# Performance work log

Hardware: AMD Instinct MI355X
Metric: run time of the kernel (lower is better)

The kernel has to match this reference:

```python
import jax, jax.numpy as jnp
import numpy as np


def mesa_head(xh, yh, qh, lam):
    # xh = per-head 'inputs' (v_proj output), yh = 'targets' (k_proj output),
    # qh = queries; all [T, d]. lam is this head's scalar lambda.
    T, d = xh.shape
    init_inv = jnp.eye(d, dtype=xh.dtype) * lam

    def step(inv, tok):
        x_t, q_t = tok
        Hx = inv @ x_t                      # [d]   (cur_inverse @ x)
        xH = x_t @ inv                      # [d]   (x^T @ cur_inverse)
        denom = 1.0 + x_t @ Hx              # scalar: forward=1 + x^T H x
        new_inv = inv - jnp.outer(Hx, xH) / denom   # Sherman-Morrison rank-1 update
        return new_inv, new_inv @ q_t       # pred_t = S_t @ q_t

    _, preds = jax.lax.scan(step, init_inv, (xh, qh))  # preds: [T, d]

    # scaled_dot_product_attention(preds, xh, yh) with masked=True,
    # use_softmax=False, normalization=False: tril-masked linear attention.
    logits = preds @ xh.T                               # [T, T]
    mask = jnp.tril(jnp.ones((T, T), dtype=bool))
    logits = jnp.where(mask, logits, jnp.zeros((), dtype=logits.dtype))
    return logits @ yh                                  # [T, d]


def reference(x, Wq, Wk, Wv, Wo, lambdas):
    B, T, E = x.shape
    H = lambdas.shape[0]
    d = Wq.shape[1] // H
    q = (x @ Wq).reshape(B, T, H, d)   # query_heads
    k = (x @ Wk).reshape(B, T, H, d)   # target_heads
    v = (x @ Wv).reshape(B, T, H, d)   # input_heads
    # Original call: mesa(input_heads, target_heads, query_heads, lambdas, norm)
    over_batch = jax.vmap(mesa_head, in_axes=(0, 0, 0, None))
    over_heads = jax.vmap(over_batch, in_axes=(2, 2, 2, 0), out_axes=-1)
    mesa_out = over_heads(v, k, q, lambdas)             # [B, T, d, H]
    # Faithful to original: reshape combines (d, H) in that order before o_proj.
    out = mesa_out.reshape(B, T, H * d) @ Wo            # [B, T, E]
    return out


def setup_inputs() -> dict:
    key = jax.random.key(0)
    ks = jax.random.split(key, 6)
    B, T, E, H, d = 2, 1024, 512, 8, 64
    s_in = 1.0 / np.sqrt(E).astype(np.float32)
    s_out = 1.0 / np.sqrt(H * d).astype(np.float32)
    return {
        "x": jax.random.normal(ks[0], (B, T, E), dtype=jnp.float32),
        "Wq": jax.random.normal(ks[1], (E, H * d), dtype=jnp.float32) * s_in,
        "Wk": jax.random.normal(ks[2], (E, H * d), dtype=jnp.float32) * s_in,
        "Wv": jax.random.normal(ks[3], (E, H * d), dtype=jnp.float32) * s_in,
        "Wo": jax.random.normal(ks[4], (H * d, E), dtype=jnp.float32) * s_out,
        "lambdas": jnp.ones((H,), dtype=jnp.float32),
    }
```

## Files before the change

kernel.cpp:

```cpp
#include <hip/hip_runtime.h>

#define T_SEQ 1024
#define DH 64
#define NH 8
#define NB 2
#define EMB 512
#define CS 32
#define NCH 32
#define ACH 16
#define NCHAIN 16

typedef __attribute__((ext_vector_type(8))) short bf16x8;
typedef __attribute__((ext_vector_type(4))) float f32x4;

__device__ __forceinline__ int swz4(int r, int c4) {
    return r * 16 + ((c4 ^ (r >> 2)) & 15);
}

__device__ __forceinline__ void fma4(float4& o, float s, const float4& b) {
    o.x += s * b.x; o.y += s * b.y; o.z += s * b.z; o.w += s * b.w;
}

__device__ __forceinline__ ushort f2bf(float f) {
    unsigned u = __float_as_uint(f);
    return (ushort)((u + 0x7FFFu + ((u >> 16) & 1u)) >> 16);
}
__device__ __forceinline__ float bf2f(ushort h) {
    return __uint_as_float(((unsigned)h) << 16);
}
__device__ __forceinline__ void split2(float f, ushort& hi, ushort& lo) {
    hi = f2bf(f);
    lo = f2bf(f - bf2f(hi));
}

__global__ __launch_bounds__(256) void prep_qkv(
    const float* __restrict__ x, const float* __restrict__ W0,
    const float* __restrict__ W1, const float* __restrict__ W2,
    ushort* __restrict__ x_hi, ushort* __restrict__ x_lo,
    ushort* __restrict__ Wt_hi, ushort* __restrict__ Wt_lo) {
    int zz = blockIdx.z;
    int t = threadIdx.x;
    __shared__ float T[64][65];
    if (zz < 3) {
        const float* W = (zz == 0) ? W0 : (zz == 1) ? W1 : W2;
        ushort* hi = Wt_hi + (size_t)zz * 262144;
        ushort* lo = Wt_lo + (size_t)zz * 262144;
        int kk0 = blockIdx.x * 64, n0 = blockIdx.y * 64;
#pragma unroll
        for (int i = 0; i < 4; ++i) {
            int rl = i * 16 + (t >> 4);
            float4 vv = *(const float4*)&W[(size_t)(kk0 + rl) * 512 + n0 + (t & 15) * 4];
            T[rl][(t & 15) * 4 + 0] = vv.x;
            T[rl][(t & 15) * 4 + 1] = vv.y;
            T[rl][(t & 15) * 4 + 2] = vv.z;
            T[rl][(t & 15) * 4 + 3] = vv.w;
        }
        __syncthreads();
        int nl = t >> 2, kl = (t & 3) * 16;
#pragma unroll
        for (int j4 = 0; j4 < 4; ++j4) {
            ushort4 h4, l4;
            split2(T[kl + j4 * 4 + 0][nl], h4.x, l4.x);
            split2(T[kl + j4 * 4 + 1][nl], h4.y, l4.y);
            split2(T[kl + j4 * 4 + 2][nl], h4.z, l4.z);
            split2(T[kl + j4 * 4 + 3][nl], h4.w, l4.w);
            size_t dst = (size_t)(n0 + nl) * 512 + kk0 + kl + j4 * 4;
            *(ushort4*)&hi[dst] = h4;
            *(ushort4*)&lo[dst] = l4;
        }
    } else {
        int bid = blockIdx.y * 8 + blockIdx.x;
        const float4* in = (const float4*)x;
        ushort4* hi = (ushort4*)x_hi;
        ushort4* lo = (ushort4*)x_lo;
#pragma unroll
        for (int i = 0; i < 16; ++i) {
            int id = (bid * 16 + i) * 256 + t;
            float4 xv = in[id];
            ushort4 h, l;
            split2(xv.x, h.x, l.x);
            split2(xv.y, h.y, l.y);
            split2(xv.z, h.z, l.z);
            split2(xv.w, h.w, l.w);
            hi[id] = h;
            lo[id] = l;
        }
    }
}

__global__ __launch_bounds__(256) void prep_out(
    const float* __restrict__ Wo, const float4* __restrict__ ao,
    ushort* __restrict__ Wot_hi, ushort* __restrict__ Wot_lo,
    ushort4* __restrict__ A2_hi, ushort4* __restrict__ A2_lo) {
    int t = threadIdx.x;
    __shared__ float T[64][65];
    if (blockIdx.z == 0) {
        int kk0 = blockIdx.x * 64, n0 = blockIdx.y * 64;
#pragma unroll
        for (int i = 0; i < 4; ++i) {
            int rl = i * 16 + (t >> 4);
            int rs = rl * 8 + (kk0 >> 6);
            float4 vv = *(const float4*)&Wo[(size_t)rs * 512 + n0 + (t & 15) * 4];
            T[rl][(t & 15) * 4 + 0] = vv.x;
            T[rl][(t & 15) * 4 + 1] = vv.y;
            T[rl][(t & 15) * 4 + 2] = vv.z;
            T[rl][(t & 15) * 4 + 3] = vv.w;
        }
        __syncthreads();
        int nl = t >> 2, kl = (t & 3) * 16;
#pragma unroll
        for (int j4 = 0; j4 < 4; ++j4) {
            ushort4 h4, l4;
            split2(T[kl + j4 * 4 + 0][nl], h4.x, l4.x);
            split2(T[kl + j4 * 4 + 1][nl], h4.y, l4.y);
            split2(T[kl + j4 * 4 + 2][nl], h4.z, l4.z);
            split2(T[kl + j4 * 4 + 3][nl], h4.w, l4.w);
            size_t dst = (size_t)(n0 + nl) * 512 + kk0 + kl + j4 * 4;
            *(ushort4*)&Wot_hi[dst] = h4;
            *(ushort4*)&Wot_lo[dst] = l4;
        }
    } else {
        int bid = blockIdx.y * 8 + blockIdx.x;
#pragma unroll
        for (int i = 0; i < 16; ++i) {
            int id = (bid * 16 + i) * 256 + t;
            int chain = id >> 14;
            int tt = (id >> 4) & 1023;
            int d4 = id & 15;
            float4 xv = ao[id];
            int mrow = ((chain >> 3) << 10) + tt;
            int dst = mrow * 128 + ((chain & 7) << 4) + d4;
            ushort4 h, l;
            split2(xv.x, h.x, l.x);
            split2(xv.y, h.y, l.y);
            split2(xv.z, h.z, l.z);
            split2(xv.w, h.w, l.w);
            A2_hi[dst] = h;
            A2_lo[dst] = l;
        }
    }
}

template <int MODE>
__global__ __launch_bounds__(256) void mfma_gemm(
    const ushort* __restrict__ Ahi, const ushort* __restrict__ Alo,
    const ushort* __restrict__ Bth, const ushort* __restrict__ Btl,
    float* __restrict__ o0, float* __restrict__ o1, float* __restrict__ o2) {
    int bm = blockIdx.x, bn = blockIdx.y, zz = blockIdx.z;
    const ushort* Bh = Bth + (size_t)zz * 262144;
    const ushort* Bl = Btl + (size_t)zz * 262144;
    float* out = (MODE == 0) ? ((zz == 0) ? o0 : (zz == 1) ? o1 : o2) : o0;

    __shared__ ushort Ash[128 * 40];
    __shared__ ushort Asl[128 * 40];
    __shared__ ushort Bsh[64 * 40];
    __shared__ ushort Bsl[64 * 40];

    int tid = threadIdx.x;
    int lane = tid & 63, wid = tid >> 6;
    int wm = wid >> 1, wn = wid & 1;
    int fr = lane & 15, fk = (lane >> 4) * 8;
    int sr = tid >> 2, sc = (tid & 3) * 8;

    f32x4 zero = {0.f, 0.f, 0.f, 0.f};
    f32x4 acc[4][2];
#pragma unroll
    for (int f = 0; f < 4; ++f)
#pragma unroll
        for (int g = 0; g < 2; ++g) acc[f][g] = zero;

    const ushort* gAh = Ahi + (size_t)(bm * 128 + sr) * 512 + sc;
    const ushort* gAl = Alo + (size_t)(bm * 128 + sr) * 512 + sc;
    const ushort* gBh = Bh + (size_t)(bn * 64 + sr) * 512 + sc;
    const ushort* gBl = Bl + (size_t)(bn * 64 + sr) * 512 + sc;

    for (int k0 = 0; k0 < 512; k0 += 32) {
        uint4 a0 = *(const uint4*)(gAh + k0);
        uint4 a1 = *(const uint4*)(gAh + 64 * 512 + k0);
        uint4 a2 = *(const uint4*)(gAl + k0);
        uint4 a3 = *(const uint4*)(gAl + 64 * 512 + k0);
        uint4 b0 = *(const uint4*)(gBh + k0);
        uint4 b1 = *(const uint4*)(gBl + k0);
        __syncthreads();
        *(uint4*)&Ash[sr * 40 + sc] = a0;
        *(uint4*)&Ash[(sr + 64) * 40 + sc] = a1;
        *(uint4*)&Asl[sr * 40 + sc] = a2;
        *(uint4*)&Asl[(sr + 64) * 40 + sc] = a3;
        *(uint4*)&Bsh[sr * 40 + sc] = b0;
        *(uint4*)&Bsl[sr * 40 + sc] = b1;
        __syncthreads();
        bf16x8 ah[4], al[4], bh[2], blo[2];
#pragma unroll
        for (int f = 0; f < 4; ++f) {
            int r = wm * 64 + f * 16 + fr;
            ah[f] = *(const bf16x8*)&Ash[r * 40 + fk];
            al[f] = *(const bf16x8*)&Asl[r * 40 + fk];
        }
#pragma unroll
        for (int g = 0; g < 2; ++g) {
            int r = wn * 32 + g * 16 + fr;
            bh[g] = *(const bf16x8*)&Bsh[r * 40 + fk];
            blo[g] = *(const bf16x8*)&Bsl[r * 40 + fk];
        }
#pragma unroll
        for (int f = 0; f < 4; ++f)
#pragma unroll
            for (int g = 0; g < 2; ++g) {
                acc[f][g] = __builtin_amdgcn_mfma_f32_16x16x32_bf16(
                    ah[f], bh[g], acc[f][g], 0, 0, 0);
                acc[f][g] = __builtin_amdgcn_mfma_f32_16x16x32_bf16(
                    ah[f], blo[g], acc[f][g], 0, 0, 0);
                acc[f][g] = __builtin_amdgcn_mfma_f32_16x16x32_bf16(
                    al[f], bh[g], acc[f][g], 0, 0, 0);
            }
    }

    int rbase = (lane >> 4) * 4;
#pragma unroll
    for (int f = 0; f < 4; ++f)
#pragma unroll
        for (int g = 0; g < 2; ++g)
#pragma unroll
            for (int j = 0; j < 4; ++j) {
                int m = bm * 128 + wm * 64 + f * 16 + rbase + j;
                int n = bn * 64 + wn * 32 + g * 16 + (lane & 15);
                float val = acc[f][g][j];
                if (MODE == 0) {
                    int b = m >> 10, tt = m & 1023;
                    int h = n >> 6, d = n & 63;
                    out[(((size_t)(b * 8 + h) * 1024 + tt) << 6) + d] = val;
                } else {
                    out[(size_t)m * 512 + n] = val;
                }
            }
}

__global__ __launch_bounds__(256) void gram_kernel(
    const float* __restrict__ v, float* __restrict__ g) {
    int chain = blockIdx.x, chunk = blockIdx.y;
    const float* X = v + ((size_t)chain * T_SEQ + chunk * CS) * DH;
    __shared__ float Xs[CS * 64];
    int tid = threadIdx.x;
#pragma unroll
    for (int i = 0; i < (CS * 16) / 256; ++i)
        ((float4*)Xs)[i * 256 + tid] = ((const float4*)X)[i * 256 + tid];
    __syncthreads();

    int tx = tid & 15, ty = tid >> 4;
    float acc[4][4];
#pragma unroll
    for (int i = 0; i < 4; ++i)
#pragma unroll
        for (int j = 0; j < 4; ++j) acc[i][j] = 0.f;

#pragma unroll 4
    for (int t = 0; t < CS; ++t) {
        float a_[4], b_[4];
#pragma unroll
        for (int i = 0; i < 4; ++i) a_[i] = Xs[t * 64 + ty * 4 + i];
#pragma unroll
        for (int j = 0; j < 4; ++j) b_[j] = Xs[t * 64 + tx * 4 + j];
#pragma unroll
        for (int i = 0; i < 4; ++i)
#pragma unroll
            for (int j = 0; j < 4; ++j) acc[i][j] += a_[i] * b_[j];
    }

    float* gp = g + ((size_t)chain * NCH + chunk) * 4096;
#pragma unroll
    for (int i = 0; i < 4; ++i)
        *(float4*)(gp + (ty * 4 + i) * 64 + tx * 4) =
            make_float4(acc[i][0], acc[i][1], acc[i][2], acc[i][3]);
}

__global__ __launch_bounds__(256) void prefix_kernel(float* __restrict__ g) {
    int gid = blockIdx.x * 256 + threadIdx.x;
    int chain = gid >> 12, elem = gid & 4095;
    float* p = g + (size_t)chain * NCH * 4096 + elem;
    float vals[NCH];
#pragma unroll
    for (int c = 0; c < NCH; ++c) vals[c] = p[(size_t)c * 4096];
    float run = 0.f;
#pragma unroll
    for (int c = 0; c < NCH; ++c) {
        float t = vals[c];
        vals[c] = run;
        run += t;
    }
#pragma unroll
    for (int c = 0; c < NCH; ++c) p[(size_t)c * 4096] = vals[c];
}

__global__ __launch_bounds__(256) void invscan(
    const float* __restrict__ g, const float* __restrict__ v,
    const float* __restrict__ q, const float* __restrict__ lambdas,
    float* __restrict__ preds) {
    int blk = blockIdx.x;
    int chain = blk >> 5, chunk = blk & 31;
    int tid = threadIdx.x;
    int row = tid >> 2, ch = tid & 3, wav = tid >> 6;
    float lam = lambdas[chain & (NH - 1)];

    __shared__ float rbuf[2][64];
    __shared__ float sbuf[2][64];
    __shared__ float Xs[CS * 64];
    __shared__ float Qs[CS * 64];
    __shared__ float Po[CS * 64];
    __shared__ float red[2][6][4];

    float m[16];
    {
        const float4* gp = (const float4*)(g + ((size_t)chain * NCH + chunk) * 4096);
#pragma unroll
        for (int i = 0; i < 4; ++i) {
            float4 t4 = gp[row * 16 + ch * 4 + i];
            m[i * 4 + 0] = t4.x; m[i * 4 + 1] = t4.y;
            m[i * 4 + 2] = t4.z; m[i * 4 + 3] = t4.w;
        }
    }
#pragma unroll
    for (int i = 0; i < 16; ++i)
        if (ch * 16 + i == row) m[i] += lam;

    const float4* vb = (const float4*)(v + ((size_t)chain * T_SEQ + chunk * CS) * DH);
    const float4* qb = (const float4*)(q + ((size_t)chain * T_SEQ + chunk * CS) * DH);
    ((float4*)Xs)[tid] = vb[tid];
    ((float4*)Xs)[256 + tid] = vb[256 + tid];
    ((float4*)Qs)[tid] = qb[tid];
    ((float4*)Qs)[256 + tid] = qb[256 + tid];

    if (row == 0) {
#pragma unroll
        for (int i = 0; i < 4; ++i)
            ((float4*)rbuf[0])[ch * 4 + i] =
                make_float4(m[i * 4], m[i * 4 + 1], m[i * 4 + 2], m[i * 4 + 3]);
    }
    if (row == 1) {
#pragma unroll
        for (int i = 0; i < 4; ++i)
            ((float4*)sbuf[0])[ch * 4 + i] =
                make_float4(m[i * 4], m[i * 4 + 1], m[i * 4 + 2], m[i * 4 + 3]);
    }
    __syncthreads();

    const int colbase = ch * 16;

    for (int pp = 0; pp < 32; ++pp) {
        const int p = 2 * pp;
        const float* rb = rbuf[pp & 1];
        const float* sb = sbuf[pp & 1];
        float r_[16], s_[16];
#pragma unroll
        for (int i = 0; i < 4; ++i) {
            float4 t4 = ((const float4*)rb)[ch * 4 + i];
            r_[i * 4] = t4.x; r_[i * 4 + 1] = t4.y;
            r_[i * 4 + 2] = t4.z; r_[i * 4 + 3] = t4.w;
            float4 u4 = ((const float4*)sb)[ch * 4 + i];
            s_[i * 4] = u4.x; s_[i * 4 + 1] = u4.y;
            s_[i * 4 + 2] = u4.z; s_[i * 4 + 3] = u4.w;
        }
        float rp = rb[p], rp2 = rb[p + 1], sp2 = sb[p + 1];
        float gr = rb[row], gs = sb[row];
        float i1 = 1.f / rp;
        float al = rp2 * i1;
        float i2 = 1.f / (sp2 - al * rp2);
        float c0, ca, cb;
        if (row == p) {
            c0 = 0.f; ca = i1 + al * al * i2; cb = -al * i2;
        } else if (row == p + 1) {
            c0 = 0.f; ca = -al * i2; cb = i2;
        } else {
            float b2 = (gs - al * gr) * i2;
            c0 = 1.f; ca = al * b2 - gr * i1; cb = -b2;
        }
#pragma unroll
        for (int i = 0; i < 16; ++i) {
            float upd = c0 * m[i] + ca * r_[i] + cb * s_[i];
            int col = colbase + i;
            upd = (col == p) ? -ca : upd;
            upd = (col == p + 1) ? -cb : upd;
            m[i] = upd;
        }
        if (pp < 31) {
            if (row == p + 2) {
#pragma unroll
                for (int i = 0; i < 4; ++i)
                    ((float4*)rbuf[(pp + 1) & 1])[ch * 4 + i] =
                        make_float4(m[i * 4], m[i * 4 + 1], m[i * 4 + 2], m[i * 4 + 3]);
            }
            if (row == p + 3) {
#pragma unroll
                for (int i = 0; i < 4; ++i)
                    ((float4*)sbuf[(pp + 1) & 1])[ch * 4 + i] =
                        make_float4(m[i * 4], m[i * 4 + 1], m[i * 4 + 2], m[i * 4 + 3]);
            }
        }
        __syncthreads();
    }

    for (int tp = 0; tp < 16; ++tp) {
        const int ta = 2 * tp, tb2 = 2 * tp + 1;
        const int par = tp & 1;
        float pu = 0.f, pw = 0.f, pza = 0.f, pzb = 0.f;
#pragma unroll
        for (int i = 0; i < 4; ++i) {
            float4 xa = ((const float4*)(Xs + ta * 64))[ch * 4 + i];
            float4 xb = ((const float4*)(Xs + tb2 * 64))[ch * 4 + i];
            float4 qa = ((const float4*)(Qs + ta * 64))[ch * 4 + i];
            float4 q4 = ((const float4*)(Qs + tb2 * 64))[ch * 4 + i];
            pu += m[i * 4] * xa.x + m[i * 4 + 1] * xa.y + m[i * 4 + 2] * xa.z + m[i * 4 + 3] * xa.w;
            pw += m[i * 4] * xb.x + m[i * 4 + 1] * xb.y + m[i * 4 + 2] * xb.z + m[i * 4 + 3] * xb.w;
            pza += m[i * 4] * qa.x + m[i * 4 + 1] * qa.y + m[i * 4 + 2] * qa.z + m[i * 4 + 3] * qa.w;
            pzb += m[i * 4] * q4.x + m[i * 4 + 1] * q4.y + m[i * 4 + 2] * q4.z + m[i * 4 + 3] * q4.w;
        }
        pu += __shfl_xor(pu, 1); pu += __shfl_xor(pu, 2);
        pw += __shfl_xor(pw, 1); pw += __shfl_xor(pw, 2);
        pza += __shfl_xor(pza, 1); pza += __shfl_xor(pza, 2);
        pzb += __shfl_xor(pzb, 1); pzb += __shfl_xor(pzb, 2);
        float u = -pu, w = -pw, za = -pza, zb = -pzb;
        if (ch == 0) rbuf[par][row] = u;
        if (ch == 1) sbuf[par][row] = w;
        float a_ = Xs[ta * 64 + row], b_ = Xs[tb2 * 64 + row];
        float qa_ = Qs[ta * 64 + row], qb_ = Qs[tb2 * 64 + row];
        float d0 = a_ * u, d1 = b_ * u, d2 = b_ * w;
        float d3 = qa_ * u, d4 = qb_ * u, d5 = qb_ * w;
#pragma unroll
        for (int off = 32; off; off >>= 1) {
            d0 += __shfl_xor(d0, off); d1 += __shfl_xor(d1, off);
            d2 += __shfl_xor(d2, off); d3 += __shfl_xor(d3, off);
            d4 += __shfl_xor(d4, off); d5 += __shfl_xor(d5, off);
        }
        if ((tid & 63) == 0) {
            red[par][0][wav] = d0; red[par][1][wav] = d1; red[par][2][wav] = d2;
            red[par][3][wav] = d3; red[par][4][wav] = d4; red[par][5][wav] = d5;
        }
        __syncthreads();
        float saa = 0.25f * (red[par][0][0] + red[par][0][1] + red[par][0][2] + red[par][0][3]);
        float sab = 0.25f * (red[par][1][0] + red[par][1][1] + red[par][1][2] + red[par][1][3]);
        float sbb = 0.25f * (red[par][2][0] + red[par][2][1] + red[par][2][2] + red[par][2][3]);
        float c1  = 0.25f * (red[par][3][0] + red[par][3][1] + red[par][3][2] + red[par][3][3]);
        float c2  = 0.25f * (red[par][4][0] + red[par][4][1] + red[par][4][2] + red[par][4][3]);
        float c3  = 0.25f * (red[par][5][0] + red[par][5][1] + red[par][5][2] + red[par][5][3]);
        float k1 = 1.f / (1.f + saa);
        float al2 = sab * k1;
        float k2 = 1.f / (1.f + sbb - sab * al2);
        float vr = w - al2 * u;
        if (ch == 0) Po[ta * 64 + row] = za - (c1 * k1) * u;
        if (ch == 1) Po[tb2 * 64 + row] = zb - (c2 * k1) * u - (k2 * (c3 - al2 * c2)) * vr;
        float cu = k1 * u - al2 * k2 * vr;
        float cw = k2 * vr;
#pragma unroll
        for (int i = 0; i < 4; ++i) {
            float4 uj = ((const float4*)rbuf[par])[ch * 4 + i];
            float4 wj = ((const float4*)sbuf[par])[ch * 4 + i];
            m[i * 4 + 0] += cu * uj.x + cw * wj.x;
            m[i * 4 + 1] += cu * uj.y + cw * wj.y;
            m[i * 4 + 2] += cu * uj.z + cw * wj.z;
            m[i * 4 + 3] += cu * uj.w + cw * wj.w;
        }
    }
    __syncthreads();

    float4* po4 = (float4*)(preds + ((size_t)chain * T_SEQ + chunk * CS) * DH);
    po4[tid] = ((const float4*)Po)[tid];
    po4[256 + tid] = ((const float4*)Po)[256 + tid];
}

__global__ __launch_bounds__(256) void kv_gram(
    const float* __restrict__ V, const float* __restrict__ Kv,
    float* __restrict__ D) {
    int chain = blockIdx.x, ck = blockIdx.y;
    __shared__ float Vs[64 * 64];
    __shared__ float Ks2[64 * 64];
    int tid = threadIdx.x;
    const float4* Vb = (const float4*)(V + ((size_t)chain * T_SEQ + ck * 64) * DH);
    const float4* Kb = (const float4*)(Kv + ((size_t)chain * T_SEQ + ck * 64) * DH);
#pragma unroll
    for (int i = 0; i < 4; ++i) {
        ((float4*)Vs)[i * 256 + tid] = Vb[i * 256 + tid];
        ((float4*)Ks2)[i * 256 + tid] = Kb[i * 256 + tid];
    }
    __syncthreads();

    int tx = tid & 15, ty = tid >> 4;
    float acc[4][4];
#pragma unroll
    for (int i = 0; i < 4; ++i)
#pragma unroll
        for (int j = 0; j < 4; ++j) acc[i][j] = 0.f;

#pragma unroll 4
    for (int t = 0; t < 64; ++t) {
        float a_[4], b_[4];
#pragma unroll
        for (int i = 0; i < 4; ++i) a_[i] = Vs[t * 64 + ty * 4 + i];
#pragma unroll
        for (int j = 0; j < 4; ++j) b_[j] = Ks2[t * 64 + tx * 4 + j];
#pragma unroll
        for (int i = 0; i < 4; ++i)
#pragma unroll
            for (int j = 0; j < 4; ++j) acc[i][j] += a_[i] * b_[j];
    }

    float* dp = D + ((size_t)chain * ACH + ck) * 4096;
#pragma unroll
    for (int i = 0; i < 4; ++i)
        *(float4*)(dp + (ty * 4 + i) * 64 + tx * 4) =
            make_float4(acc[i][0], acc[i][1], acc[i][2], acc[i][3]);
}

__global__ __launch_bounds__(256) void kv_prefix(float* __restrict__ d) {
    int gid = blockIdx.x * 256 + threadIdx.x;
    int chain = gid >> 12, elem = gid & 4095;
    float* p = d + (size_t)chain * ACH * 4096 + elem;
    float vals[ACH];
#pragma unroll
    for (int c = 0; c < ACH; ++c) vals[c] = p[(size_t)c * 4096];
    float run = 0.f;
#pragma unroll
    for (int c = 0; c < ACH; ++c) {
        float t = vals[c];
        vals[c] = run;
        run += t;
    }
#pragma unroll
    for (int c = 0; c < ACH; ++c) p[(size_t)c * 4096] = vals[c];
}

__global__ __launch_bounds__(256) void attn_chunk(
    const float* __restrict__ P, const float* __restrict__ V,
    const float* __restrict__ Kv, const float* __restrict__ C,
    float* __restrict__ O) {
    int ck = blockIdx.x, bh = blockIdx.y;
    int tid = threadIdx.x, tx = tid & 15, ty = tid >> 4;

    __shared__ float4 Ps[64 * 16];
    __shared__ float4 Bs[64 * 16];
    __shared__ float4 Ks[64 * 16];

    int lr = tid >> 2, lc = tid & 3;
    const float4* Pb = (const float4*)(P + ((size_t)bh * T_SEQ + ck * 64) * DH);
    const float4* Vb = (const float4*)(V + ((size_t)bh * T_SEQ + ck * 64) * DH);
    const float4* Kb = (const float4*)(Kv + ((size_t)bh * T_SEQ + ck * 64) * DH);
    const float4* Cb = (const float4*)(C + ((size_t)bh * ACH + ck) * 4096);
#pragma unroll
    for (int i = 0; i < 4; ++i) {
        Ps[swz4(lr, lc + i * 4)] = Pb[lr * 16 + lc + i * 4];
        Bs[swz4(lr, lc + i * 4)] = Cb[lr * 16 + lc + i * 4];
        Ks[swz4(lr, lc + i * 4)] = Kb[lr * 16 + lc + i * 4];
    }

    float4 o[4];
    o[0] = o[1] = o[2] = o[3] = make_float4(0.f, 0.f, 0.f, 0.f);
    __syncthreads();

    const float* Pf = (const float*)Ps;
#pragma unroll 4
    for (int j = 0; j < 64; ++j) {
        float4 b4 = Bs[swz4(j, tx)];
#pragma unroll
        for (int i = 0; i < 4; ++i) {
            float s = Pf[swz4(ty * 4 + i, j >> 2) * 4 + (j & 3)];
            fma4(o[i], s, b4);
        }
    }
    __syncthreads();

#pragma unroll
    for (int i = 0; i < 4; ++i)
        Bs[swz4(lr, lc + i * 4)] = Vb[lr * 16 + lc + i * 4];
    __syncthreads();

    float4 sa[4][4];
#pragma unroll
    for (int i = 0; i < 4; ++i)
#pragma unroll
        for (int j = 0; j < 4; ++j) sa[i][j] = make_float4(0.f, 0.f, 0.f, 0.f);
#pragma unroll
    for (int d4 = 0; d4 < 16; ++d4) {
        float4 a[4], b[4];
#pragma unroll
        for (int i = 0; i < 4; ++i) a[i] = Ps[swz4(ty * 4 + i, d4)];
#pragma unroll
        for (int j = 0; j < 4; ++j) b[j] = Bs[swz4(tx * 4 + j, d4)];
#pragma unroll
        for (int i = 0; i < 4; ++i)
#pragma unroll
            for (int j = 0; j < 4; ++j) {
                sa[i][j].x += a[i].x * b[j].x;
                sa[i][j].y += a[i].y * b[j].y;
                sa[i][j].z += a[i].z * b[j].z;
                sa[i][j].w += a[i].w * b[j].w;
            }
    }
    __syncthreads();

#pragma unroll
    for (int i = 0; i < 4; ++i) {
        int m = ty * 4 + i;
        float sv[4];
#pragma unroll
        for (int j = 0; j < 4; ++j) {
            float s = sa[i][j].x + sa[i][j].y + sa[i][j].z + sa[i][j].w;
            if ((tx * 4 + j) > m) s = 0.f;
            sv[j] = s;
        }
        Bs[swz4(m, tx)] = make_float4(sv[0], sv[1], sv[2], sv[3]);
    }
    __syncthreads();

    const float* Sf = (const float*)Bs;
#pragma unroll 4
    for (int j = 0; j < 64; ++j) {
        float4 b4 = Ks[swz4(j, tx)];
#pragma unroll
        for (int i = 0; i < 4; ++i) {
            float s = Sf[swz4(ty * 4 + i, j >> 2) * 4 + (j & 3)];
            fma4(o[i], s, b4);
        }
    }

#pragma unroll
    for (int i = 0; i < 4; ++i) {
        float* dst = O + ((size_t)bh * T_SEQ + ck * 64 + ty * 4 + i) * DH + tx * 4;
        *(float4*)dst = o[i];
    }
}

extern "C" void kernel_launch(void* const* d_in, const int* in_sizes, int n_in,
                              void* d_out, int out_size, void* d_ws, size_t ws_size,
                              hipStream_t stream) {
    const float* x = (const float*)d_in[0];
    const float* Wq = (const float*)d_in[1];
    const float* Wk = (const float*)d_in[2];
    const float* Wv = (const float*)d_in[3];
    const float* Wo = (const float*)d_in[4];
    const float* lambdas = (const float*)d_in[5];
    float* out = (float*)d_out;

    float* ws = (float*)d_ws;
    const size_t SZ = (size_t)NB * NH * T_SEQ * DH;
    float* q = ws;
    float* k = ws + SZ;
    float* v = ws + 2 * SZ;
    float* preds = ws + 3 * SZ;
    ushort* x_hi = (ushort*)(ws + 3 * SZ);
    ushort* x_lo = (ushort*)(ws + 3 * SZ + SZ / 2);
    ushort* A2_hi = x_hi;
    ushort* A2_lo = x_lo;
    float* g = ws + 4 * SZ;
    ushort* Wt_hi = (ushort*)(ws + 4 * SZ);
    ushort* Wt_lo = (ushort*)(ws + 4 * SZ + 393216);
    float* dbuf = g;
    float* ao = g + SZ;
    ushort* Wot_hi = (ushort*)(ws + 4 * SZ);
    ushort* Wot_lo = (ushort*)(ws + 4 * SZ + 131072);

    prep_qkv<<<dim3(8, 8, 4), 256, 0, stream>>>(x, Wq, Wk, Wv,
                                                x_hi, x_lo, Wt_hi, Wt_lo);
    mfma_gemm<0><<<dim3(16, 8, 3), 256, 0, stream>>>(
        x_hi, x_lo, Wt_hi, Wt_lo, q, k, v);
    gram_kernel<<<dim3(NCHAIN, NCH), 256, 0, stream>>>(v, g);
    prefix_kernel<<<dim3(256), 256, 0, stream>>>(g);
    invscan<<<dim3(NCHAIN * NCH), 256, 0, stream>>>(g, v, q, lambdas, preds);
    kv_gram<<<dim3(NCHAIN, ACH), 256, 0, stream>>>(v, k, dbuf);
    kv_prefix<<<dim3(256), 256, 0, stream>>>(dbuf);
    attn_chunk<<<dim3(ACH, NCHAIN), 256, 0, stream>>>(preds, v, k, dbuf, ao);
    prep_out<<<dim3(8, 8, 2), 256, 0, stream>>>(Wo, (const float4*)ao,
                                                Wot_hi, Wot_lo,
                                                (ushort4*)A2_hi, (ushort4*)A2_lo);
    mfma_gemm<1><<<dim3(16, 8, 1), 256, 0, stream>>>(
        A2_hi, A2_lo, Wot_hi, Wot_lo, out, out, out);
}
```

Baseline: 137.8 us.

## Run invscan as a single wavefront with register-resident rows and readlane broadcasts

The per-chunk inverse scan kernel moves from a 256-thread block, where four threads share each matrix row and pivot rows pass through shared memory with barriers, to one 64-lane wavefront. Each lane now holds a full row of 64 floats, and pivot and row values are broadcast with readlane. This removes every __syncthreads and the cross-wave reductions in both the Gauss-Jordan inversion and the per-token rank-1 update loop. In exchange each lane does four times the arithmetic, uses about 64 more registers, and the inversion now pivots one column at a time instead of two.

```diff
diff --git a/kernel.cpp b/kernel.cpp
--- a/kernel.cpp
+++ b/kernel.cpp
@@ -31,6 +31,10 @@
 __device__ __forceinline__ void split2(float f, ushort& hi, ushort& lo) {
     hi = f2bf(f);
     lo = f2bf(f - bf2f(hi));
+}
+
+__device__ __forceinline__ float rlane(float x, int l) {
+    return __int_as_float(__builtin_amdgcn_readlane(__float_as_int(x), l));
 }
 
 __global__ __launch_bounds__(256) void prep_qkv(
@@ -291,179 +295,89 @@
     for (int c = 0; c < NCH; ++c) p[(size_t)c * 4096] = vals[c];
 }
 
-__global__ __launch_bounds__(256) void invscan(
+__global__ __launch_bounds__(64) void invscan(
     const float* __restrict__ g, const float* __restrict__ v,
     const float* __restrict__ q, const float* __restrict__ lambdas,
     float* __restrict__ preds) {
     int blk = blockIdx.x;
     int chain = blk >> 5, chunk = blk & 31;
-    int tid = threadIdx.x;
-    int row = tid >> 2, ch = tid & 3, wav = tid >> 6;
+    int lane = threadIdx.x;
     float lam = lambdas[chain & (NH - 1)];
 
-    __shared__ float rbuf[2][64];
-    __shared__ float sbuf[2][64];
     __shared__ float Xs[CS * 64];
     __shared__ float Qs[CS * 64];
-    __shared__ float Po[CS * 64];
-    __shared__ float red[2][6][4];
-
-    float m[16];
+
+    const float4* vb = (const float4*)(v + ((size_t)chain * T_SEQ + chunk * CS) * DH);
+    const float4* qb = (const float4*)(q + ((size_t)chain * T_SEQ + chunk * CS) * DH);
+#pragma unroll
+    for (int i = 0; i < 8; ++i) {
+        ((float4*)Xs)[i * 64 + lane] = vb[i * 64 + lane];
+        ((float4*)Qs)[i * 64 + lane] = qb[i * 64 + lane];
+    }
+
+    float m[64];
     {
         const float4* gp = (const float4*)(g + ((size_t)chain * NCH + chunk) * 4096);
 #pragma unroll
-        for (int i = 0; i < 4; ++i) {
-            float4 t4 = gp[row * 16 + ch * 4 + i];
+        for (int i = 0; i < 16; ++i) {
+            float4 t4 = gp[lane * 16 + i];
             m[i * 4 + 0] = t4.x; m[i * 4 + 1] = t4.y;
             m[i * 4 + 2] = t4.z; m[i * 4 + 3] = t4.w;
         }
     }
 #pragma unroll
-    for (int i = 0; i < 16; ++i)
-        if (ch * 16 + i == row) m[i] += lam;
-
-    const float4* vb = (const float4*)(v + ((size_t)chain * T_SEQ + chunk * CS) * DH);
-    const float4* qb = (const float4*)(q + ((size_t)chain * T_SEQ + chunk * CS) * DH);
-    ((float4*)Xs)[tid] = vb[tid];
-    ((float4*)Xs)[256 + tid] = vb[256 + tid];
-    ((float4*)Qs)[tid] = qb[tid];
-    ((float4*)Qs)[256 + tid] = qb[256 + tid];
-
-    if (row == 0) {
-#pragma unroll
-        for (int i = 0; i < 4; ++i)
-            ((float4*)rbuf[0])[ch * 4 + i] =
-                make_float4(m[i * 4], m[i * 4 + 1], m[i * 4 + 2], m[i * 4 + 3]);
-    }
-    if (row == 1) {
-#pragma unroll
-        for (int i = 0; i < 4; ++i)
-            ((float4*)sbuf[0])[ch * 4 + i] =
-                make_float4(m[i * 4], m[i * 4 + 1], m[i * 4 + 2], m[i * 4 + 3]);
-    }
-    __syncthreads();
-
-    const int colbase = ch * 16;
-
-    for (int pp = 0; pp < 32; ++pp) {
-        const int p = 2 * pp;
-        const float* rb = rbuf[pp & 1];
-        const float* sb = sbuf[pp & 1];
-        float r_[16], s_[16];
-#pragma unroll
-        for (int i = 0; i < 4; ++i) {
-            float4 t4 = ((const float4*)rb)[ch * 4 + i];
-            r_[i * 4] = t4.x; r_[i * 4 + 1] = t4.y;
-            r_[i * 4 + 2] = t4.z; r_[i * 4 + 3] = t4.w;
-            float4 u4 = ((const float4*)sb)[ch * 4 + i];
-            s_[i * 4] = u4.x; s_[i * 4 + 1] = u4.y;
-            s_[i * 4 + 2] = u4.z; s_[i * 4 + 3] = u4.w;
-        }
-        float rp = rb[p], rp2 = rb[p + 1], sp2 = sb[p + 1];
-        float gr = rb[row], gs = sb[row];
-        float i1 = 1.f / rp;
-        float al = rp2 * i1;
-        float i2 = 1.f / (sp2 - al * rp2);
-        float c0, ca, cb;
-        if (row == p) {
-            c0 = 0.f; ca = i1 + al * al * i2; cb = -al * i2;
-        } else if (row == p + 1) {
-            c0 = 0.f; ca = -al * i2; cb = i2;
-        } else {
-            float b2 = (gs - al * gr) * i2;
-            c0 = 1.f; ca = al * b2 - gr * i1; cb = -b2;
-        }
+    for (int j = 0; j < 64; ++j)
+        m[j] += (j == lane) ? lam : 0.f;
+
+#pragma unroll
+    for (int p = 0; p < 64; ++p) {
+        float diag = rlane(m[p], p);
+        float ipiv = 1.f / diag;
+        float gcv = m[p];
+        bool isp = (lane == p);
+        float beta = gcv * ipiv;
+        float c2 = isp ? ipiv : -beta;
+#pragma unroll
+        for (int j = 0; j < 64; ++j) {
+            float sj = rlane(m[j], p);
+            float base = isp ? 0.f : m[j];
+            m[j] = fmaf(c2, sj, base);
+        }
+        m[p] = isp ? -ipiv : beta;
+    }
+
+    float* pb = preds + ((size_t)chain * T_SEQ + chunk * CS) * DH;
+    for (int t = 0; t < CS; ++t) {
+        const float4* x4p = (const float4*)(Xs + t * 64);
+        const float4* q4p = (const float4*)(Qs + t * 64);
+        float hx = 0.f, hq = 0.f;
 #pragma unroll
         for (int i = 0; i < 16; ++i) {
-            float upd = c0 * m[i] + ca * r_[i] + cb * s_[i];
-            int col = colbase + i;
-            upd = (col == p) ? -ca : upd;
-            upd = (col == p + 1) ? -cb : upd;
-            m[i] = upd;
-        }
-        if (pp < 31) {
-            if (row == p + 2) {
-#pragma unroll
-                for (int i = 0; i < 4; ++i)
-                    ((float4*)rbuf[(pp + 1) & 1])[ch * 4 + i] =
-                        make_float4(m[i * 4], m[i * 4 + 1], m[i * 4 + 2], m[i * 4 + 3]);
-            }
-            if (row == p + 3) {
-#pragma unroll
-                for (int i = 0; i < 4; ++i)
-                    ((float4*)sbuf[(pp + 1) & 1])[ch * 4 + i] =
-                        make_float4(m[i * 4], m[i * 4 + 1], m[i * 4 + 2], m[i * 4 + 3]);
-            }
-        }
-        __syncthreads();
-    }
-
-    for (int tp = 0; tp < 16; ++tp) {
-        const int ta = 2 * tp, tb2 = 2 * tp + 1;
-        const int par = tp & 1;
-        float pu = 0.f, pw = 0.f, pza = 0.f, pzb = 0.f;
-#pragma unroll
-        for (int i = 0; i < 4; ++i) {
-            float4 xa = ((const float4*)(Xs + ta * 64))[ch * 4 + i];
-            float4 xb = ((const float4*)(Xs + tb2 * 64))[ch * 4 + i];
-            float4 qa = ((const float4*)(Qs + ta * 64))[ch * 4 + i];
-            float4 q4 = ((const float4*)(Qs + tb2 * 64))[ch * 4 + i];
-            pu += m[i * 4] * xa.x + m[i * 4 + 1] * xa.y + m[i * 4 + 2] * xa.z + m[i * 4 + 3] * xa.w;
-            pw += m[i * 4] * xb.x + m[i * 4 + 1] * xb.y + m[i * 4 + 2] * xb.z + m[i * 4 + 3] * xb.w;
-            pza += m[i * 4] * qa.x + m[i * 4 + 1] * qa.y + m[i * 4 + 2] * qa.z + m[i * 4 + 3] * qa.w;
-            pzb += m[i * 4] * q4.x + m[i * 4 + 1] * q4.y + m[i * 4 + 2] * q4.z + m[i * 4 + 3] * q4.w;
-        }
-        pu += __shfl_xor(pu, 1); pu += __shfl_xor(pu, 2);
-        pw += __shfl_xor(pw, 1); pw += __shfl_xor(pw, 2);
-        pza += __shfl_xor(pza, 1); pza += __shfl_xor(pza, 2);
-        pzb += __shfl_xor(pzb, 1); pzb += __shfl_xor(pzb, 2);
-        float u = -pu, w = -pw, za = -pza, zb = -pzb;
-        if (ch == 0) rbuf[par][row] = u;
-        if (ch == 1) sbuf[par][row] = w;
-        float a_ = Xs[ta * 64 + row], b_ = Xs[tb2 * 64 + row];
-        float qa_ = Qs[ta * 64 + row], qb_ = Qs[tb2 * 64 + row];
-        float d0 = a_ * u, d1 = b_ * u, d2 = b_ * w;
-        float d3 = qa_ * u, d4 = qb_ * u, d5 = qb_ * w;
+            float4 x4 = x4p[i];
+            float4 q4 = q4p[i];
+            hx += m[i * 4 + 0] * x4.x + m[i * 4 + 1] * x4.y +
+                  m[i * 4 + 2] * x4.z + m[i * 4 + 3] * x4.w;
+            hq += m[i * 4 + 0] * q4.x + m[i * 4 + 1] * q4.y +
+                  m[i * 4 + 2] * q4.z + m[i * 4 + 3] * q4.w;
+        }
+        float Hx = -hx, Hq = -hq;
+
+        float xr = Xs[t * 64 + lane];
+        float qr = Qs[t * 64 + lane];
+        float s1 = xr * Hx, s2 = qr * Hx;
 #pragma unroll
         for (int off = 32; off; off >>= 1) {
-            d0 += __shfl_xor(d0, off); d1 += __shfl_xor(d1, off);
-            d2 += __shfl_xor(d2, off); d3 += __shfl_xor(d3, off);
-            d4 += __shfl_xor(d4, off); d5 += __shfl_xor(d5, off);
-        }
-        if ((tid & 63) == 0) {
-            red[par][0][wav] = d0; red[par][1][wav] = d1; red[par][2][wav] = d2;
-            red[par][3][wav] = d3; red[par][4][wav] = d4; red[par][5][wav] = d5;
-        }
-        __syncthreads();
-        float saa = 0.25f * (red[par][0][0] + red[par][0][1] + red[par][0][2] + red[par][0][3]);
-        float sab = 0.25f * (red[par][1][0] + red[par][1][1] + red[par][1][2] + red[par][1][3]);
-        float sbb = 0.25f * (red[par][2][0] + red[par][2][1] + red[par][2][2] + red[par][2][3]);
-        float c1  = 0.25f * (red[par][3][0] + red[par][3][1] + red[par][3][2] + red[par][3][3]);
-        float c2  = 0.25f * (red[par][4][0] + red[par][4][1] + red[par][4][2] + red[par][4][3]);
-        float c3  = 0.25f * (red[par][5][0] + red[par][5][1] + red[par][5][2] + red[par][5][3]);
-        float k1 = 1.f / (1.f + saa);
-        float al2 = sab * k1;
-        float k2 = 1.f / (1.f + sbb - sab * al2);
-        float vr = w - al2 * u;
-        if (ch == 0) Po[ta * 64 + row] = za - (c1 * k1) * u;
-        if (ch == 1) Po[tb2 * 64 + row] = zb - (c2 * k1) * u - (k2 * (c3 - al2 * c2)) * vr;
-        float cu = k1 * u - al2 * k2 * vr;
-        float cw = k2 * vr;
-#pragma unroll
-        for (int i = 0; i < 4; ++i) {
-            float4 uj = ((const float4*)rbuf[par])[ch * 4 + i];
-            float4 wj = ((const float4*)sbuf[par])[ch * 4 + i];
-            m[i * 4 + 0] += cu * uj.x + cw * wj.x;
-            m[i * 4 + 1] += cu * uj.y + cw * wj.y;
-            m[i * 4 + 2] += cu * uj.z + cw * wj.z;
-            m[i * 4 + 3] += cu * uj.w + cw * wj.w;
-        }
-    }
-    __syncthreads();
-
-    float4* po4 = (float4*)(preds + ((size_t)chain * T_SEQ + chunk * CS) * DH);
-    po4[tid] = ((const float4*)Po)[tid];
-    po4[256 + tid] = ((const float4*)Po)[256 + tid];
+            s1 += __shfl_xor(s1, off);
+            s2 += __shfl_xor(s2, off);
+        }
+        float idn = 1.f / (1.f + s1);
+        pb[(size_t)t * DH + lane] = Hq - Hx * (s2 * idn);
+
+        float coef = Hx * idn;
+#pragma unroll
+        for (int j = 0; j < 64; ++j)
+            m[j] = fmaf(coef, rlane(Hx, j), m[j]);
+    }
 }
 
 __global__ __launch_bounds__(256) void kv_gram(
@@ -662,7 +576,7 @@
         x_hi, x_lo, Wt_hi, Wt_lo, q, k, v);
     gram_kernel<<<dim3(NCHAIN, NCH), 256, 0, stream>>>(v, g);
     prefix_kernel<<<dim3(256), 256, 0, stream>>>(g);
-    invscan<<<dim3(NCHAIN * NCH), 256, 0, stream>>>(g, v, q, lambdas, preds);
+    invscan<<<dim3(NCHAIN * NCH), 64, 0, stream>>>(g, v, q, lambdas, preds);
     kv_gram<<<dim3(NCHAIN, ACH), 256, 0, stream>>>(v, k, dbuf);
     kv_prefix<<<dim3(256), 256, 0, stream>>>(dbuf);
     attn_chunk<<<dim3(ACH, NCHAIN), 256, 0, stream>>>(preds, v, k, dbuf, ao);
```

Result: slower. 160.7 us (+16.6%).

## Fuse output bf16 split into attention epilogue and Wo prep into kv_gram

Applied to the files above, without the earlier changes.

Removes the prep_out kernel. attn_chunk now writes its output directly as hi/lo bf16 pairs in the GEMM A-operand layout, and the Wo transpose/split runs as extra blocks of the kv_gram launch. The invscan inner loops are also fully unrolled, and the per-element column-select masking is replaced with a single conditional write of the pivot columns. This saves one launch plus an fp32 round trip of the attention output, at the cost of more register pressure and larger code from the unrolling, and it relocates workspace buffers (Wot now aliases q at the workspace start).

```diff
diff --git a/kernel.cpp b/kernel.cpp
--- a/kernel.cpp
+++ b/kernel.cpp
@@ -84,59 +84,6 @@
             split2(xv.w, h.w, l.w);
             hi[id] = h;
             lo[id] = l;
-        }
-    }
-}
-
-__global__ __launch_bounds__(256) void prep_out(
-    const float* __restrict__ Wo, const float4* __restrict__ ao,
-    ushort* __restrict__ Wot_hi, ushort* __restrict__ Wot_lo,
-    ushort4* __restrict__ A2_hi, ushort4* __restrict__ A2_lo) {
-    int t = threadIdx.x;
-    __shared__ float T[64][65];
-    if (blockIdx.z == 0) {
-        int kk0 = blockIdx.x * 64, n0 = blockIdx.y * 64;
-#pragma unroll
-        for (int i = 0; i < 4; ++i) {
-            int rl = i * 16 + (t >> 4);
-            int rs = rl * 8 + (kk0 >> 6);
-            float4 vv = *(const float4*)&Wo[(size_t)rs * 512 + n0 + (t & 15) * 4];
-            T[rl][(t & 15) * 4 + 0] = vv.x;
-            T[rl][(t & 15) * 4 + 1] = vv.y;
-            T[rl][(t & 15) * 4 + 2] = vv.z;
-            T[rl][(t & 15) * 4 + 3] = vv.w;
-        }
-        __syncthreads();
-        int nl = t >> 2, kl = (t & 3) * 16;
-#pragma unroll
-        for (int j4 = 0; j4 < 4; ++j4) {
-            ushort4 h4, l4;
-            split2(T[kl + j4 * 4 + 0][nl], h4.x, l4.x);
-            split2(T[kl + j4 * 4 + 1][nl], h4.y, l4.y);
-            split2(T[kl + j4 * 4 + 2][nl], h4.z, l4.z);
-            split2(T[kl + j4 * 4 + 3][nl], h4.w, l4.w);
-            size_t dst = (size_t)(n0 + nl) * 512 + kk0 + kl + j4 * 4;
-            *(ushort4*)&Wot_hi[dst] = h4;
-            *(ushort4*)&Wot_lo[dst] = l4;
-        }
-    } else {
-        int bid = blockIdx.y * 8 + blockIdx.x;
-#pragma unroll
-        for (int i = 0; i < 16; ++i) {
-            int id = (bid * 16 + i) * 256 + t;
-            int chain = id >> 14;
-            int tt = (id >> 4) & 1023;
-            int d4 = id & 15;
-            float4 xv = ao[id];
-            int mrow = ((chain >> 3) << 10) + tt;
-            int dst = mrow * 128 + ((chain & 7) << 4) + d4;
-            ushort4 h, l;
-            split2(xv.x, h.x, l.x);
-            split2(xv.y, h.y, l.y);
-            split2(xv.z, h.z, l.z);
-            split2(xv.w, h.w, l.w);
-            A2_hi[dst] = h;
-            A2_lo[dst] = l;
         }
     }
 }
@@ -343,8 +290,7 @@
     }
     __syncthreads();
 
-    const int colbase = ch * 16;
-
+#pragma unroll
     for (int pp = 0; pp < 32; ++pp) {
         const int p = 2 * pp;
         const float* rb = rbuf[pp & 1];
@@ -374,12 +320,10 @@
             c0 = 1.f; ca = al * b2 - gr * i1; cb = -b2;
         }
 #pragma unroll
-        for (int i = 0; i < 16; ++i) {
-            float upd = c0 * m[i] + ca * r_[i] + cb * s_[i];
-            int col = colbase + i;
-            upd = (col == p) ? -ca : upd;
-            upd = (col == p + 1) ? -cb : upd;
-            m[i] = upd;
+        for (int i = 0; i < 16; ++i) m[i] = c0 * m[i] + ca * r_[i] + cb * s_[i];
+        if (ch == (p >> 4)) {
+            m[p & 15] = -ca;
+            m[(p & 15) + 1] = -cb;
         }
         if (pp < 31) {
             if (row == p + 2) {
@@ -398,6 +342,7 @@
         __syncthreads();
     }
 
+#pragma unroll
     for (int tp = 0; tp < 16; ++tp) {
         const int ta = 2 * tp, tb2 = 2 * tp + 1;
         const int par = tp & 1;
@@ -466,47 +411,77 @@
     po4[256 + tid] = ((const float4*)Po)[256 + tid];
 }
 
-__global__ __launch_bounds__(256) void kv_gram(
+__global__ __launch_bounds__(256) void kvg_wot(
     const float* __restrict__ V, const float* __restrict__ Kv,
-    float* __restrict__ D) {
-    int chain = blockIdx.x, ck = blockIdx.y;
-    __shared__ float Vs[64 * 64];
-    __shared__ float Ks2[64 * 64];
+    float* __restrict__ D, const float* __restrict__ Wo,
+    ushort* __restrict__ Wot_hi, ushort* __restrict__ Wot_lo) {
+    __shared__ float smem[8192];
     int tid = threadIdx.x;
-    const float4* Vb = (const float4*)(V + ((size_t)chain * T_SEQ + ck * 64) * DH);
-    const float4* Kb = (const float4*)(Kv + ((size_t)chain * T_SEQ + ck * 64) * DH);
-#pragma unroll
-    for (int i = 0; i < 4; ++i) {
-        ((float4*)Vs)[i * 256 + tid] = Vb[i * 256 + tid];
-        ((float4*)Ks2)[i * 256 + tid] = Kb[i * 256 + tid];
-    }
-    __syncthreads();
-
-    int tx = tid & 15, ty = tid >> 4;
-    float acc[4][4];
-#pragma unroll
-    for (int i = 0; i < 4; ++i)
-#pragma unroll
-        for (int j = 0; j < 4; ++j) acc[i][j] = 0.f;
+    if (blockIdx.y < 16) {
+        int chain = blockIdx.x, ck = blockIdx.y;
+        float* Vs = smem;
+        float* Ks2 = smem + 4096;
+        const float4* Vb = (const float4*)(V + ((size_t)chain * T_SEQ + ck * 64) * DH);
+        const float4* Kb = (const float4*)(Kv + ((size_t)chain * T_SEQ + ck * 64) * DH);
+#pragma unroll
+        for (int i = 0; i < 4; ++i) {
+            ((float4*)Vs)[i * 256 + tid] = Vb[i * 256 + tid];
+            ((float4*)Ks2)[i * 256 + tid] = Kb[i * 256 + tid];
+        }
+        __syncthreads();
+
+        int tx = tid & 15, ty = tid >> 4;
+        float acc[4][4];
+#pragma unroll
+        for (int i = 0; i < 4; ++i)
+#pragma unroll
+            for (int j = 0; j < 4; ++j) acc[i][j] = 0.f;
 
 #pragma unroll 4
-    for (int t = 0; t < 64; ++t) {
-        float a_[4], b_[4];
-#pragma unroll
-        for (int i = 0; i < 4; ++i) a_[i] = Vs[t * 64 + ty * 4 + i];
-#pragma unroll
-        for (int j = 0; j < 4; ++j) b_[j] = Ks2[t * 64 + tx * 4 + j];
+        for (int t = 0; t < 64; ++t) {
+            float a_[4], b_[4];
+#pragma unroll
+            for (int i = 0; i < 4; ++i) a_[i] = Vs[t * 64 + ty * 4 + i];
+#pragma unroll
+            for (int j = 0; j < 4; ++j) b_[j] = Ks2[t * 64 + tx * 4 + j];
+#pragma unroll
+            for (int i = 0; i < 4; ++i)
+#pragma unroll
+                for (int j = 0; j < 4; ++j) acc[i][j] += a_[i] * b_[j];
+        }
+
+        float* dp = D + ((size_t)chain * ACH + ck) * 4096;
 #pragma unroll
         for (int i = 0; i < 4; ++i)
-#pragma unroll
-            for (int j = 0; j < 4; ++j) acc[i][j] += a_[i] * b_[j];
-    }
-
-    float* dp = D + ((size_t)chain * ACH + ck) * 4096;
-#pragma unroll
-    for (int i = 0; i < 4; ++i)
-        *(float4*)(dp + (ty * 4 + i) * 64 + tx * 4) =
-            make_float4(acc[i][0], acc[i][1], acc[i][2], acc[i][3]);
+            *(float4*)(dp + (ty * 4 + i) * 64 + tx * 4) =
+                make_float4(acc[i][0], acc[i][1], acc[i][2], acc[i][3]);
+    } else {
+        int wb = blockIdx.x * 4 + (blockIdx.y - 16);
+        int kk0 = (wb >> 3) * 64, n0 = (wb & 7) * 64;
+#pragma unroll
+        for (int i = 0; i < 4; ++i) {
+            int rl = i * 16 + (tid >> 4);
+            int rs = rl * 8 + (kk0 >> 6);
+            float4 vv = *(const float4*)&Wo[(size_t)rs * 512 + n0 + (tid & 15) * 4];
+            smem[rl * 65 + (tid & 15) * 4 + 0] = vv.x;
+            smem[rl * 65 + (tid & 15) * 4 + 1] = vv.y;
+            smem[rl * 65 + (tid & 15) * 4 + 2] = vv.z;
+            smem[rl * 65 + (tid & 15) * 4 + 3] = vv.w;
+        }
+        __syncthreads();
+        int nl = tid >> 2, kl = (tid & 3) * 16;
+#pragma unroll
+        for (int j4 = 0; j4 < 4; ++j4) {
+            ushort4 h4, l4;
+            split2(smem[(kl + j4 * 4 + 0) * 65 + nl], h4.x, l4.x);
+            split2(smem[(kl + j4 * 4 + 1) * 65 + nl], h4.y, l4.y);
+            split2(smem[(kl + j4 * 4 + 2) * 65 + nl], h4.z, l4.z);
+            split2(smem[(kl + j4 * 4 + 3) * 65 + nl], h4.w, l4.w);
+            size_t dst = (size_t)(n0 + nl) * 512 + kk0 + kl + j4 * 4;
+            *(ushort4*)&Wot_hi[dst] = h4;
+            *(ushort4*)&Wot_lo[dst] = l4;
+        }
+    }
 }
 
 __global__ __launch_bounds__(256) void kv_prefix(float* __restrict__ d) {
@@ -530,7 +505,7 @@
 __global__ __launch_bounds__(256) void attn_chunk(
     const float* __restrict__ P, const float* __restrict__ V,
     const float* __restrict__ Kv, const float* __restrict__ C,
-    float* __restrict__ O) {
+    ushort* __restrict__ A2_hi, ushort* __restrict__ A2_lo) {
     int ck = blockIdx.x, bh = blockIdx.y;
     int tid = threadIdx.x, tx = tid & 15, ty = tid >> 4;
 
@@ -620,10 +595,18 @@
         }
     }
 
+    int kkb = ((bh & 7) << 6) + tx * 4;
 #pragma unroll
     for (int i = 0; i < 4; ++i) {
-        float* dst = O + ((size_t)bh * T_SEQ + ck * 64 + ty * 4 + i) * DH + tx * 4;
-        *(float4*)dst = o[i];
+        int t = ck * 64 + ty * 4 + i;
+        size_t mrow = (size_t)((bh >> 3) << 10) + t;
+        ushort4 h, l;
+        split2(o[i].x, h.x, l.x);
+        split2(o[i].y, h.y, l.y);
+        split2(o[i].z, h.z, l.z);
+        split2(o[i].w, h.w, l.w);
+        *(ushort4*)&A2_hi[mrow * 512 + kkb] = h;
+        *(ushort4*)&A2_lo[mrow * 512 + kkb] = l;
     }
 }
 
@@ -646,15 +629,14 @@
     float* preds = ws + 3 * SZ;
     ushort* x_hi = (ushort*)(ws + 3 * SZ);
     ushort* x_lo = (ushort*)(ws + 3 * SZ + SZ / 2);
-    ushort* A2_hi = x_hi;
-    ushort* A2_lo = x_lo;
     float* g = ws + 4 * SZ;
     ushort* Wt_hi = (ushort*)(ws + 4 * SZ);
     ushort* Wt_lo = (ushort*)(ws + 4 * SZ + 393216);
     float* dbuf = g;
-    float* ao = g + SZ;
-    ushort* Wot_hi = (ushort*)(ws + 4 * SZ);
-    ushort* Wot_lo = (ushort*)(ws + 4 * SZ + 131072);
+    ushort* A2_hi = (ushort*)(ws + 5 * SZ);
+    ushort* A2_lo = (ushort*)(ws + 5 * SZ + SZ / 2);
+    ushort* Wot_hi = (ushort*)ws;
+    ushort* Wot_lo = (ushort*)(ws + 131072);
 
     prep_qkv<<<dim3(8, 8, 4), 256, 0, stream>>>(x, Wq, Wk, Wv,
                                                 x_hi, x_lo, Wt_hi, Wt_lo);
@@ -663,12 +645,11 @@
     gram_kernel<<<dim3(NCHAIN, NCH), 256, 0, stream>>>(v, g);
     prefix_kernel<<<dim3(256), 256, 0, stream>>>(g);
     invscan<<<dim3(NCHAIN * NCH), 256, 0, stream>>>(g, v, q, lambdas, preds);
-    kv_gram<<<dim3(NCHAIN, ACH), 256, 0, stream>>>(v, k, dbuf);
+    kvg_wot<<<dim3(NCHAIN, ACH + 4), 256, 0, stream>>>(v, k, dbuf, Wo,
+                                                       Wot_hi, Wot_lo);
     kv_prefix<<<dim3(256), 256, 0, stream>>>(dbuf);
-    attn_chunk<<<dim3(ACH, NCHAIN), 256, 0, stream>>>(preds, v, k, dbuf, ao);
-    prep_out<<<dim3(8, 8, 2), 256, 0, stream>>>(Wo, (const float4*)ao,
-                                                Wot_hi, Wot_lo,
-                                                (ushort4*)A2_hi, (ushort4*)A2_lo);
+    attn_chunk<<<dim3(ACH, NCHAIN), 256, 0, stream>>>(preds, v, k, dbuf,
+                                                      A2_hi, A2_lo);
     mfma_gemm<1><<<dim3(16, 8, 1), 256, 0, stream>>>(
         A2_hi, A2_lo, Wot_hi, Wot_lo, out, out, out);
 }
```

New measurement: 129.0 us. -6.4%, faster.
